# Kernel tuning notes

Hardware: AMD Instinct MI355X
Metric: run time of the kernel (lower is better)

The kernel has to match this reference:

```python
import jax, jax.numpy as jnp
import numpy as np

HIDDEN = 2048
N_HEADS = 8
N_KV_HEADS = 1
HEAD_DIM = 256
ROPE_THETA = 10000.0
B, S = 2, 2048


def setup_inputs() -> dict:
    key = jax.random.key(0)
    ks = jax.random.split(key, 6)
    sc = 0.02
    hidden_states = jax.random.normal(ks[0], (B, S, HIDDEN), dtype=jnp.float32)
    position_ids = jnp.broadcast_to(jnp.arange(S, dtype=jnp.int64 if jax.config.jax_enable_x64 else jnp.int32), (B, S))
    # additive causal mask: 0 on/below diagonal, large negative above
    causal = jnp.tril(jnp.ones((S, S), dtype=bool))
    attention_mask = jnp.where(causal, 0.0, -1e9).astype(jnp.float32)[None, None, :, :]
    attention_mask = jnp.broadcast_to(attention_mask, (B, 1, S, S))
    Wq = jax.random.normal(ks[1], (HIDDEN, N_HEADS * HEAD_DIM), dtype=jnp.float32) * sc
    Wk = jax.random.normal(ks[2], (HIDDEN, N_KV_HEADS * HEAD_DIM), dtype=jnp.float32) * sc
    Wv = jax.random.normal(ks[3], (HIDDEN, N_KV_HEADS * HEAD_DIM), dtype=jnp.float32) * sc
    Wo = jax.random.normal(ks[4], (N_HEADS * HEAD_DIM, HIDDEN), dtype=jnp.float32) * sc
    return {"hidden_states": hidden_states, "position_ids": position_ids,
            "attention_mask": attention_mask, "Wq": Wq, "Wk": Wk, "Wv": Wv, "Wo": Wo}


def _rotate_half(x):
    x1, x2 = jnp.split(x, 2, axis=-1)
    return jnp.concatenate([-x2, x1], axis=-1)


def _rope_cos_sin(position_ids, dtype):
    # inv_freq: [head_dim/2]
    inv_freq = 1.0 / (ROPE_THETA ** (jnp.arange(0, HEAD_DIM, 2, dtype=jnp.float32) / HEAD_DIM))
    # freqs: [B, S, head_dim/2]
    freqs = position_ids.astype(jnp.float32)[:, :, None] * inv_freq[None, None, :]
    emb = jnp.concatenate([freqs, freqs], axis=-1)  # [B, S, head_dim]
    return jnp.cos(emb).astype(dtype), jnp.sin(emb).astype(dtype)


def reference(hidden_states, position_ids, attention_mask, Wq, Wk, Wv, Wo):
    b, s, _ = hidden_states.shape
    # projections (bias=False)
    q = (hidden_states @ Wq).reshape(b, s, N_HEADS, HEAD_DIM).transpose(0, 2, 1, 3)      # [B,H,S,D]
    k = (hidden_states @ Wk).reshape(b, s, N_KV_HEADS, HEAD_DIM).transpose(0, 2, 1, 3)   # [B,Hk,S,D]
    v = (hidden_states @ Wv).reshape(b, s, N_KV_HEADS, HEAD_DIM).transpose(0, 2, 1, 3)
    cos, sin = _rope_cos_sin(position_ids, hidden_states.dtype)  # [B,S,D]
    cos, sin = cos[:, None], sin[:, None]  # [B,1,S,D]
    q = q * cos + _rotate_half(q) * sin
    k = k * cos + _rotate_half(k) * sin
    # repeat_kv for GQA
    n_rep = N_HEADS // N_KV_HEADS
    k = jnp.repeat(k, n_rep, axis=1)  # [B,H,S,D]
    v = jnp.repeat(v, n_rep, axis=1)
    scale = HEAD_DIM ** -0.5
    scores = jnp.einsum('bhqd,bhkd->bhqk', q, k) * scale + attention_mask
    attn_weights = jax.nn.softmax(scores.astype(jnp.float32), axis=-1).astype(q.dtype)
    attn_out = jnp.einsum('bhqk,bhkd->bhqd', attn_weights, v)
    attn_out = attn_out.transpose(0, 2, 1, 3).reshape(b, s, N_HEADS * HEAD_DIM)
    out = attn_out @ Wo
    return out, attn_weights
```

## Files before the change

kernel.cpp:

```cpp
#include <hip/hip_runtime.h>
#include <hip/hip_bf16.h>
#include <math.h>

typedef __attribute__((ext_vector_type(4))) float f32x4;
typedef __attribute__((ext_vector_type(8))) __bf16 bf16x8;
typedef __attribute__((ext_vector_type(8))) unsigned short u16x8;
typedef __attribute__((ext_vector_type(4))) unsigned short u16x4;

#define HID    2048
#define NHEADS 8
#define HDIM   256
#define SEQ    2048
#define BATCH  2
#define ROWS   (BATCH*SEQ)
#define QKVN   (NHEADS*HDIM + 2*HDIM)
#define NBH    (BATCH*NHEADS)

typedef __attribute__((address_space(1))) const void gvoid_t;
typedef __attribute__((address_space(3))) void lvoid_t;

__device__ __forceinline__ void gload16(const void* g, void* l){
  __builtin_amdgcn_global_load_lds((gvoid_t*)g, (lvoid_t*)l, 16, 0, 0);
}

__device__ __forceinline__ float bf2f(unsigned short u){
  union { unsigned int i; float f; } x; x.i = ((unsigned int)u) << 16; return x.f;
}
__device__ __forceinline__ unsigned short f2bf(float f){
  union { float f; unsigned int i; } x; x.f = f;
  unsigned int u = x.i;
  return (unsigned short)((u + 0x7FFFu + ((u >> 16) & 1u)) >> 16);
}

__global__ __launch_bounds__(256)
void k_f32_to_bf16(const float* __restrict__ src, unsigned short* __restrict__ dst){
  long i = ((long)blockIdx.x * 256 + threadIdx.x) * 16;
  f32x4 x0 = *(const f32x4*)(src + i);
  f32x4 x1 = *(const f32x4*)(src + i + 4);
  f32x4 x2 = *(const f32x4*)(src + i + 8);
  f32x4 x3 = *(const f32x4*)(src + i + 12);
  u16x8 w0, w1;
  #pragma unroll
  for (int j = 0; j < 4; ++j){
    w0[j]   = f2bf(x0[j]);
    w0[4+j] = f2bf(x1[j]);
    w1[j]   = f2bf(x2[j]);
    w1[4+j] = f2bf(x3[j]);
  }
  *(u16x8*)(dst + i)     = w0;
  *(u16x8*)(dst + i + 8) = w1;
}

__global__ __launch_bounds__(256)
void k_transpose(const float* __restrict__ src, unsigned short* __restrict__ dst,
                 int srcCols, int dstLd){
  __shared__ float t[32][33];
  int bx = blockIdx.x * 32;
  int by = blockIdx.y * 32;
  int tx = threadIdx.x & 31, ty = threadIdx.x >> 5;
  #pragma unroll
  for (int i = 0; i < 4; ++i){
    int rr = ty + i*8;
    t[rr][tx] = src[(long)(by + rr)*srcCols + bx + tx];
  }
  __syncthreads();
  #pragma unroll
  for (int i = 0; i < 4; ++i){
    int rr = ty + i*8;
    dst[(long)(bx + rr)*dstLd + by + tx] = f2bf(t[tx][rr]);
  }
}

__global__ __launch_bounds__(256)
void k_rope(const unsigned short* __restrict__ qkv, const int* __restrict__ pos_ids,
            unsigned short* __restrict__ Qb, unsigned short* __restrict__ Kb){
  int row = blockIdx.x;
  float pos = (float)pos_ids[row];
  int tid = threadIdx.x;
  const unsigned short* r = qkv + (long)row * QKVN;

  #pragma unroll
  for (int it = 0; it < 4; ++it){
    int p = it*256 + tid;
    int d = p & 127, h = p >> 7;
    int col = h*HDIM + d;
    float inv = exp2f((float)d * -0.10381025296523132f);
    float ang = pos * inv;
    float sn, cs; sincosf(ang, &sn, &cs);
    float x0 = bf2f(r[col]), x1 = bf2f(r[col + 128]);
    Qb[(long)row*HID + col]       = f2bf(x0*cs - x1*sn);
    Qb[(long)row*HID + col + 128] = f2bf(x1*cs + x0*sn);
  }
  if (tid < 128){
    int d = tid;
    float inv = exp2f((float)d * -0.10381025296523132f);
    float ang = pos * inv;
    float sn, cs; sincosf(ang, &sn, &cs);
    float x0 = bf2f(r[HID + d]), x1 = bf2f(r[HID + d + 128]);
    Kb[(long)row*HDIM + d]       = f2bf(x0*cs - x1*sn);
    Kb[(long)row*HDIM + d + 128] = f2bf(x1*cs + x0*sn);
  }
}

__global__ __launch_bounds__(256)
void k_vt(const unsigned short* __restrict__ qkvb, unsigned short* __restrict__ VT){
  __shared__ unsigned short t[32][34];
  int d0 = blockIdx.x * 32, s0 = blockIdx.y * 32, b = blockIdx.z;
  int tx = threadIdx.x & 31, ty = threadIdx.x >> 5;
  #pragma unroll
  for (int i = 0; i < 4; ++i){
    int rr = ty + i*8;
    t[rr][tx] = qkvb[(long)(b*SEQ + s0 + rr)*QKVN + HID + HDIM + d0 + tx];
  }
  __syncthreads();
  #pragma unroll
  for (int i = 0; i < 4; ++i){
    int dd = ty + i*8;
    VT[((long)b*HDIM + d0 + dd)*SEQ + s0 + tx] = t[tx][dd];
  }
}

__global__ __launch_bounds__(512, 4)
void k_fused(const unsigned short* __restrict__ Qb, const unsigned short* __restrict__ Kb,
             const unsigned short* __restrict__ VT, float* __restrict__ S,
             unsigned short* __restrict__ AOb){
  int bh = blockIdx.x, b = bh >> 3, h = bh & 7;
  int ss = 31 - (int)blockIdx.y;
  int qbase = ss * 64;
  int T = 2 * (ss + 1);

  float* Sh = S + (long)bh * SEQ * SEQ;
  const unsigned short* Qh = Qb + (long)b*SEQ*HID + (long)h*HDIM;
  const unsigned short* Kh = Kb + (long)b*SEQ*HDIM;
  const unsigned short* Vh = VT + (long)b*HDIM*SEQ;

  __shared__ unsigned short lK[2][32*256];
  __shared__ __bf16 lA[2][64*40];
  __shared__ float lWl[8][64];
  __shared__ float mli[64];

  int tid = threadIdx.x, lane = tid & 63, w = tid >> 6;
  int wr = w >> 1, wc = w & 1;

#define STAGE_K(kt_, buf_)                                                      \
  { _Pragma("unroll")                                                           \
    for (int t = 0; t < 2; ++t){                                                \
      int seg = w*2 + t;                                                        \
      int row = seg*2 + (lane >> 5);                                            \
      int cb  = ((lane & 31)*16) ^ ((row & 7) << 4);                            \
      gload16(Kh + (long)((kt_)*32 + row)*HDIM + (cb >> 1),                     \
              (char*)lK[buf_] + seg*1024);                                      \
    } }

#define QKT(buf_)                                                               \
  { _Pragma("unroll")                                                           \
    for (int kk = 0; kk < 8; ++kk){                                             \
      int rk = wc*16 + (lane & 15);                                             \
      bf16x8 bk = *(const bf16x8*)((const char*)lK[buf_] + rk*512 +             \
                   ((kk*64 + (lane >> 4)*16) ^ ((rk & 7) << 4)));               \
      accs = __builtin_amdgcn_mfma_f32_16x16x32_bf16(aq[kk], bk, accs, 0, 0, 0);\
    } }

  bf16x8 aq[8];
  {
    const unsigned short* qrow = Qh + (long)(qbase + wr*16 + (lane & 15))*HID + (lane >> 4)*8;
    #pragma unroll
    for (int kk = 0; kk < 8; ++kk)
      aq[kk] = *(const bf16x8*)(qrow + kk*32);
  }

  f32x4 accs;
  f32x4 acc_o[4][2];
  float oL[4];
  #pragma unroll
  for (int q = 0; q < 4; ++q){ accs[q] = 0.f; oL[q] = 0.f; }
  #pragma unroll
  for (int m = 0; m < 4; ++m)
    #pragma unroll
    for (int n = 0; n < 2; ++n)
      #pragma unroll
      for (int q = 0; q < 4; ++q) acc_o[m][n][q] = 0.f;

  STAGE_K(0, 0)
  STAGE_K(1, 1)
  asm volatile("s_waitcnt vmcnt(2)" ::: "memory");
  __builtin_amdgcn_s_barrier();
  for (int kt = 0; kt < T; ++kt){
    __builtin_amdgcn_s_setprio(1);
    QKT(kt & 1)
    __builtin_amdgcn_s_setprio(0);
    if (kt*32 + wc*16 + 15 <= qbase + wr*16){
      #pragma unroll
      for (int ri = 0; ri < 4; ++ri){
        int rowl = wr*16 + (lane >> 4)*4 + ri;
        int coll = wc*16 + (lane & 15);
        float e = __expf(accs[ri]*0.0625f - 8.0f);
        oL[ri] += e;
        lA[kt & 1][rowl*40 + coll] = (__bf16)e;
        accs[ri] = 0.f;
      }
    } else {
      #pragma unroll
      for (int ri = 0; ri < 4; ++ri){
        int rowl = wr*16 + (lane >> 4)*4 + ri;
        int coll = wc*16 + (lane & 15);
        float e = (kt*32 + coll <= qbase + rowl) ? __expf(accs[ri]*0.0625f - 8.0f) : 0.f;
        oL[ri] += e;
        lA[kt & 1][rowl*40 + coll] = (__bf16)e;
        accs[ri] = 0.f;
      }
    }
    bf16x8 vf0 = *(const bf16x8*)(Vh + (long)(w*32 +      (lane & 15))*SEQ + kt*32 + (lane >> 4)*8);
    bf16x8 vf1 = *(const bf16x8*)(Vh + (long)(w*32 + 16 + (lane & 15))*SEQ + kt*32 + (lane >> 4)*8);
    asm volatile("s_waitcnt lgkmcnt(0)" ::: "memory");
    asm volatile("s_waitcnt vmcnt(2)" ::: "memory");
    __builtin_amdgcn_s_barrier();
    if (kt + 2 < T) STAGE_K(kt + 2, kt & 1)
    __builtin_amdgcn_s_setprio(1);
    #pragma unroll
    for (int m2 = 0; m2 < 4; ++m2){
      int rq = m2*16 + (lane & 15);
      bf16x8 ap = *(const bf16x8*)&lA[kt & 1][rq*40 + (lane >> 4)*8];
      acc_o[m2][0] = __builtin_amdgcn_mfma_f32_16x16x32_bf16(ap, vf0, acc_o[m2][0], 0, 0, 0);
      acc_o[m2][1] = __builtin_amdgcn_mfma_f32_16x16x32_bf16(ap, vf1, acc_o[m2][1], 0, 0, 0);
    }
    __builtin_amdgcn_s_setprio(0);
  }

  #pragma unroll
  for (int ri = 0; ri < 4; ++ri){
    float v = oL[ri];
    #pragma unroll
    for (int off = 1; off < 16; off <<= 1) v += __shfl_xor(v, off);
    if ((lane & 15) == 0)
      lWl[w][wr*16 + (lane >> 4)*4 + ri] = v;
  }
  __syncthreads();
  if (tid < 64){
    int g = (tid >> 4) * 2;
    mli[tid] = 1.0f / (lWl[g][tid] + lWl[g+1][tid]);
  }
  __syncthreads();

  float ils[4];
  #pragma unroll
  for (int ri = 0; ri < 4; ++ri)
    ils[ri] = mli[wr*16 + (lane >> 4)*4 + ri];

  #pragma unroll
  for (int m2 = 0; m2 < 4; ++m2){
    #pragma unroll
    for (int ri = 0; ri < 4; ++ri){
      int row = m2*16 + (lane >> 4)*4 + ri;
      float il = mli[row];
      long gr = (long)b*SEQ + qbase + row;
      #pragma unroll
      for (int n = 0; n < 2; ++n){
        int col = w*32 + n*16 + (lane & 15);
        AOb[gr*HID + h*HDIM + col] = f2bf(acc_o[m2][n][ri] * il);
      }
    }
  }

  STAGE_K(0, 0)
  STAGE_K(1, 1)
  asm volatile("s_waitcnt vmcnt(2)" ::: "memory");
  __builtin_amdgcn_s_barrier();
  for (int kt = 0; kt < T; ++kt){
    __builtin_amdgcn_s_setprio(1);
    QKT(kt & 1)
    __builtin_amdgcn_s_setprio(0);
    if (kt*32 + wc*16 + 15 <= qbase + wr*16){
      #pragma unroll
      for (int ri = 0; ri < 4; ++ri){
        int rowl = wr*16 + (lane >> 4)*4 + ri;
        int coll = wc*16 + (lane & 15);
        Sh[(long)(qbase + rowl)*SEQ + kt*32 + coll] =
            __expf(accs[ri]*0.0625f - 8.0f) * ils[ri];
        accs[ri] = 0.f;
      }
    } else {
      #pragma unroll
      for (int ri = 0; ri < 4; ++ri){
        int rowl = wr*16 + (lane >> 4)*4 + ri;
        int coll = wc*16 + (lane & 15);
        float p = (kt*32 + coll <= qbase + rowl)
                  ? __expf(accs[ri]*0.0625f - 8.0f) * ils[ri] : 0.f;
        Sh[(long)(qbase + rowl)*SEQ + kt*32 + coll] = p;
        accs[ri] = 0.f;
      }
    }
    asm volatile("s_waitcnt vmcnt(4)" ::: "memory");
    __builtin_amdgcn_s_barrier();
    if (kt + 2 < T) STAGE_K(kt + 2, kt & 1)
  }

  {
    f32x4 z4; z4[0]=0.f; z4[1]=0.f; z4[2]=0.f; z4[3]=0.f;
    int row = qbase + (tid >> 3);
    for (int c = T*32 + (tid & 7)*4; c < SEQ; c += 32)
      *(f32x4*)&Sh[(long)row*SEQ + c] = z4;
  }
#undef STAGE_K
#undef QKT
}

template<int OUTF32>
__global__ __launch_bounds__(512, 1)
void gemm256(const unsigned short* __restrict__ A16, const unsigned short* __restrict__ BT,
             void* __restrict__ Cv, int lda, int ldb, int ldc, int K){
  constexpr int BM = 256, BN = 128, BK = 64;
  int m0 = blockIdx.x * BM, n0 = blockIdx.y * BN;

  __shared__ unsigned short lA[2][BM*BK];
  __shared__ unsigned short lB[2][BN*BK];

  int tid = threadIdx.x, lane = tid & 63, w = tid >> 6;
  int wr = w >> 1, wc = w & 1;
  int srow = lane >> 3;
  int vswz = ((lane & 7) ^ ((lane >> 3) & 7)) * 8;

  f32x4 acc[4][4];
  #pragma unroll
  for (int m = 0; m < 4; ++m)
    #pragma unroll
    for (int n = 0; n < 4; ++n)
      #pragma unroll
      for (int q = 0; q < 4; ++q) acc[m][n][q] = 0.f;

  int NT = K / BK;

#define STAGE256(kt_, buf_)                                                    \
  { int k0_ = (kt_) * BK;                                                      \
    _Pragma("unroll")                                                          \
    for (int t = 0; t < 4; ++t){                                               \
      int seg = w*4 + t;                                                       \
      const unsigned short* src = A16 + (long)(m0 + seg*8 + srow)*lda + k0_ + vswz; \
      gload16(src, (char*)lA[buf_] + seg*1024);                                \
    }                                                                          \
    _Pragma("unroll")                                                          \
    for (int t = 0; t < 2; ++t){                                               \
      int seg = w*2 + t;                                                       \
      const unsigned short* src = BT + (long)(n0 + seg*8 + srow)*ldb + k0_ + vswz; \
      gload16(src, (char*)lB[buf_] + seg*1024);                                \
    } }

  STAGE256(0, 0)
  STAGE256(1, 1)
  int cur = 0;

  for (int kt = 0; kt < NT; ++kt){
    if (kt < NT - 1) asm volatile("s_waitcnt vmcnt(6)" ::: "memory");
    else             asm volatile("s_waitcnt vmcnt(0)" ::: "memory");
    __builtin_amdgcn_s_barrier();

    const char* La = (const char*)lA[cur];
    const char* Lb = (const char*)lB[cur];
    __builtin_amdgcn_s_setprio(1);
    #pragma unroll
    for (int kk = 0; kk < 2; ++kk){
      bf16x8 af[4], bfr[4];
      #pragma unroll
      for (int m = 0; m < 4; ++m){
        int row = wr*64 + m*16 + (lane & 15);
        int kb = (kk*64 + (lane >> 4)*16) ^ ((row & 7) << 4);
        af[m] = *(const bf16x8*)(La + row*128 + kb);
      }
      #pragma unroll
      for (int n = 0; n < 4; ++n){
        int row = wc*64 + n*16 + (lane & 15);
        int kb = (kk*64 + (lane >> 4)*16) ^ ((row & 7) << 4);
        bfr[n] = *(const bf16x8*)(Lb + row*128 + kb);
      }
      #pragma unroll
      for (int m = 0; m < 4; ++m)
        #pragma unroll
        for (int n = 0; n < 4; ++n)
          acc[m][n] = __builtin_amdgcn_mfma_f32_16x16x32_bf16(af[m], bfr[n], acc[m][n], 0, 0, 0);
    }
    __builtin_amdgcn_s_setprio(0);
    __builtin_amdgcn_s_barrier();
    if (kt + 2 < NT) STAGE256(kt + 2, cur)
    cur ^= 1;
  }
#undef STAGE256

  #pragma unroll
  for (int m = 0; m < 4; ++m){
    #pragma unroll
    for (int ri = 0; ri < 4; ++ri){
      int orow = m0 + wr*64 + m*16 + (lane >> 4)*4 + ri;
      #pragma unroll
      for (int n = 0; n < 4; ++n){
        int ocol = n0 + wc*64 + n*16 + (lane & 15);
        float vv = acc[m][n][ri];
        if (OUTF32) ((float*)Cv)[(long)orow*ldc + ocol] = vv;
        else        ((unsigned short*)Cv)[(long)orow*ldc + ocol] = f2bf(vv);
      }
    }
  }
}

extern "C" void kernel_launch(void* const* d_in, const int* in_sizes, int n_in,
                              void* d_out, int out_size, void* d_ws, size_t ws_size,
                              hipStream_t stream){
  const float* hs  = (const float*)d_in[0];
  const int*   pos = (const int*)  d_in[1];
  const float* Wq  = (const float*)d_in[3];
  const float* Wk  = (const float*)d_in[4];
  const float* Wv  = (const float*)d_in[5];
  const float* Wo  = (const float*)d_in[6];

  float* out  = (float*)d_out;
  float* Sbuf = out + (long)ROWS * HID;

  unsigned short* wsp   = (unsigned short*)d_ws;
  unsigned short* hsb   = wsp;
  unsigned short* wqkvT = hsb   + (long)ROWS*HID;
  unsigned short* woT   = wqkvT + (long)QKVN*HID;
  unsigned short* qkvb  = woT   + (long)HID*HID;
  unsigned short* Qb    = qkvb  + (long)ROWS*QKVN;
  unsigned short* Kb    = Qb    + (long)ROWS*HID;
  unsigned short* VT    = Kb    + (long)ROWS*HDIM;
  unsigned short* AOb   = VT    + (long)BATCH*HDIM*SEQ;

  k_f32_to_bf16<<<(ROWS*HID)/(256*16), 256, 0, stream>>>(hs, hsb);
  k_transpose<<<dim3(HID/32,  HID/32), 256, 0, stream>>>(Wq, wqkvT, HID, HID);
  k_transpose<<<dim3(HDIM/32, HID/32), 256, 0, stream>>>(Wk, wqkvT + (long)HID*HID, HDIM, HID);
  k_transpose<<<dim3(HDIM/32, HID/32), 256, 0, stream>>>(Wv, wqkvT + (long)(HID+HDIM)*HID, HDIM, HID);
  k_transpose<<<dim3(HID/32,  HID/32), 256, 0, stream>>>(Wo, woT, HID, HID);

  gemm256<0><<<dim3(ROWS/256, QKVN/128), 512, 0, stream>>>(
      hsb, wqkvT, qkvb, HID, HID, QKVN, HID);

  k_rope<<<ROWS, 256, 0, stream>>>(qkvb, pos, Qb, Kb);
  k_vt<<<dim3(HDIM/32, SEQ/32, BATCH), 256, 0, stream>>>(qkvb, VT);

  k_fused<<<dim3(NBH, 32), 512, 0, stream>>>(Qb, Kb, VT, Sbuf, AOb);

  gemm256<1><<<dim3(ROWS/256, HID/128), 512, 0, stream>>>(
      AOb, woT, out, HID, HID, HID, HID);
}
```

Before: 318.4 us.

## Triple-buffer K tiles, prefetch V one step ahead, interleave block order

```diff
diff --git a/kernel.cpp b/kernel.cpp
--- a/kernel.cpp
+++ b/kernel.cpp
@@ -5,7 +5,6 @@
 typedef __attribute__((ext_vector_type(4))) float f32x4;
 typedef __attribute__((ext_vector_type(8))) __bf16 bf16x8;
 typedef __attribute__((ext_vector_type(8))) unsigned short u16x8;
-typedef __attribute__((ext_vector_type(4))) unsigned short u16x4;
 
 #define HID    2048
 #define NHEADS 8
@@ -125,7 +124,8 @@
              const unsigned short* __restrict__ VT, float* __restrict__ S,
              unsigned short* __restrict__ AOb){
   int bh = blockIdx.x, b = bh >> 3, h = bh & 7;
-  int ss = 31 - (int)blockIdx.y;
+  int y = (int)blockIdx.y;
+  int ss = (y < 16) ? (31 - y) : (y - 16);
   int qbase = ss * 64;
   int T = 2 * (ss + 1);
 
@@ -134,7 +134,7 @@
   const unsigned short* Kh = Kb + (long)b*SEQ*HDIM;
   const unsigned short* Vh = VT + (long)b*HDIM*SEQ;
 
-  __shared__ unsigned short lK[2][32*256];
+  __shared__ unsigned short lK[3][32*256];
   __shared__ __bf16 lA[2][64*40];
   __shared__ float lWl[8][64];
   __shared__ float mli[64];
@@ -168,6 +168,8 @@
     for (int kk = 0; kk < 8; ++kk)
       aq[kk] = *(const bf16x8*)(qrow + kk*32);
   }
+  const unsigned short* vb0 = Vh + (long)(w*32 +      (lane & 15))*SEQ + (lane >> 4)*8;
+  const unsigned short* vb1 = Vh + (long)(w*32 + 16 + (lane & 15))*SEQ + (lane >> 4)*8;
 
   f32x4 accs;
   f32x4 acc_o[4][2];
@@ -183,11 +185,22 @@
 
   STAGE_K(0, 0)
   STAGE_K(1, 1)
-  asm volatile("s_waitcnt vmcnt(2)" ::: "memory");
+  if (T > 2) STAGE_K(2, 2)
+  bf16x8 vc0 = *(const bf16x8*)(vb0);
+  bf16x8 vc1 = *(const bf16x8*)(vb1);
+  if (T > 2) asm volatile("s_waitcnt vmcnt(6)" ::: "memory");
+  else       asm volatile("s_waitcnt vmcnt(4)" ::: "memory");
   __builtin_amdgcn_s_barrier();
+
+  int bc = 0;
   for (int kt = 0; kt < T; ++kt){
+    bf16x8 vn0, vn1;
+    if (kt + 1 < T){
+      vn0 = *(const bf16x8*)(vb0 + (kt+1)*32);
+      vn1 = *(const bf16x8*)(vb1 + (kt+1)*32);
+    }
     __builtin_amdgcn_s_setprio(1);
-    QKT(kt & 1)
+    QKT(bc)
     __builtin_amdgcn_s_setprio(0);
     if (kt*32 + wc*16 + 15 <= qbase + wr*16){
       #pragma unroll
@@ -210,21 +223,24 @@
         accs[ri] = 0.f;
       }
     }
-    bf16x8 vf0 = *(const bf16x8*)(Vh + (long)(w*32 +      (lane & 15))*SEQ + kt*32 + (lane >> 4)*8);
-    bf16x8 vf1 = *(const bf16x8*)(Vh + (long)(w*32 + 16 + (lane & 15))*SEQ + kt*32 + (lane >> 4)*8);
     asm volatile("s_waitcnt lgkmcnt(0)" ::: "memory");
-    asm volatile("s_waitcnt vmcnt(2)" ::: "memory");
+    if (kt + 1 < T){
+      if (kt + 2 < T) asm volatile("s_waitcnt vmcnt(6)" ::: "memory");
+      else            asm volatile("s_waitcnt vmcnt(4)" ::: "memory");
+    }
     __builtin_amdgcn_s_barrier();
-    if (kt + 2 < T) STAGE_K(kt + 2, kt & 1)
+    if (kt + 3 < T) STAGE_K(kt + 3, bc)
     __builtin_amdgcn_s_setprio(1);
     #pragma unroll
     for (int m2 = 0; m2 < 4; ++m2){
       int rq = m2*16 + (lane & 15);
       bf16x8 ap = *(const bf16x8*)&lA[kt & 1][rq*40 + (lane >> 4)*8];
-      acc_o[m2][0] = __builtin_amdgcn_mfma_f32_16x16x32_bf16(ap, vf0, acc_o[m2][0], 0, 0, 0);
-      acc_o[m2][1] = __builtin_amdgcn_mfma_f32_16x16x32_bf16(ap, vf1, acc_o[m2][1], 0, 0, 0);
+      acc_o[m2][0] = __builtin_amdgcn_mfma_f32_16x16x32_bf16(ap, vc0, acc_o[m2][0], 0, 0, 0);
+      acc_o[m2][1] = __builtin_amdgcn_mfma_f32_16x16x32_bf16(ap, vc1, acc_o[m2][1], 0, 0, 0);
     }
     __builtin_amdgcn_s_setprio(0);
+    vc0 = vn0; vc1 = vn1;
+    bc = (bc == 2) ? 0 : bc + 1;
   }
 
   #pragma unroll
@@ -264,11 +280,15 @@
 
   STAGE_K(0, 0)
   STAGE_K(1, 1)
-  asm volatile("s_waitcnt vmcnt(2)" ::: "memory");
+  if (T > 2) STAGE_K(2, 2)
+  if (T > 2) asm volatile("s_waitcnt vmcnt(4)" ::: "memory");
+  else       asm volatile("s_waitcnt vmcnt(2)" ::: "memory");
   __builtin_amdgcn_s_barrier();
+
+  bc = 0;
   for (int kt = 0; kt < T; ++kt){
     __builtin_amdgcn_s_setprio(1);
-    QKT(kt & 1)
+    QKT(bc)
     __builtin_amdgcn_s_setprio(0);
     if (kt*32 + wc*16 + 15 <= qbase + wr*16){
       #pragma unroll
@@ -290,9 +310,18 @@
         accs[ri] = 0.f;
       }
     }
-    asm volatile("s_waitcnt vmcnt(4)" ::: "memory");
-    __builtin_amdgcn_s_barrier();
-    if (kt + 2 < T) STAGE_K(kt + 2, kt & 1)
+    if (kt + 1 < T){
+      if (kt == 0){
+        if (kt + 2 < T) asm volatile("s_waitcnt vmcnt(6)" ::: "memory");
+        else            asm volatile("s_waitcnt vmcnt(4)" ::: "memory");
+      } else {
+        if (kt + 2 < T) asm volatile("s_waitcnt vmcnt(10)" ::: "memory");
+        else            asm volatile("s_waitcnt vmcnt(8)" ::: "memory");
+      }
+      __builtin_amdgcn_s_barrier();
+      if (kt + 3 < T) STAGE_K(kt + 3, bc)
+    }
+    bc = (bc == 2) ? 0 : bc + 1;
   }
 
   {
```

Result: slower. 346.9 us (+9.0%).

## Shrink fused attention query tile to 32 rows with 256-thread blocks

Applied to the files above, without the earlier changes.

```diff
diff --git a/kernel.cpp b/kernel.cpp
--- a/kernel.cpp
+++ b/kernel.cpp
@@ -5,7 +5,6 @@
 typedef __attribute__((ext_vector_type(4))) float f32x4;
 typedef __attribute__((ext_vector_type(8))) __bf16 bf16x8;
 typedef __attribute__((ext_vector_type(8))) unsigned short u16x8;
-typedef __attribute__((ext_vector_type(4))) unsigned short u16x4;
 
 #define HID    2048
 #define NHEADS 8
@@ -120,14 +119,14 @@
   }
 }
 
-__global__ __launch_bounds__(512, 4)
+__global__ __launch_bounds__(256, 4)
 void k_fused(const unsigned short* __restrict__ Qb, const unsigned short* __restrict__ Kb,
              const unsigned short* __restrict__ VT, float* __restrict__ S,
              unsigned short* __restrict__ AOb){
   int bh = blockIdx.x, b = bh >> 3, h = bh & 7;
-  int ss = 31 - (int)blockIdx.y;
-  int qbase = ss * 64;
-  int T = 2 * (ss + 1);
+  int ss = 63 - (int)blockIdx.y;
+  int qbase = ss * 32;
+  int T = ss + 1;
 
   float* Sh = S + (long)bh * SEQ * SEQ;
   const unsigned short* Qh = Qb + (long)b*SEQ*HID + (long)h*HDIM;
@@ -135,17 +134,17 @@
   const unsigned short* Vh = VT + (long)b*HDIM*SEQ;
 
   __shared__ unsigned short lK[2][32*256];
-  __shared__ __bf16 lA[2][64*40];
-  __shared__ float lWl[8][64];
-  __shared__ float mli[64];
+  __shared__ __bf16 lA[2][32*40];
+  __shared__ float lWl[4][32];
+  __shared__ float mli[32];
 
   int tid = threadIdx.x, lane = tid & 63, w = tid >> 6;
-  int wr = w >> 1, wc = w & 1;
+  int wr = w & 1, wc = w >> 1;
 
 #define STAGE_K(kt_, buf_)                                                      \
   { _Pragma("unroll")                                                           \
-    for (int t = 0; t < 2; ++t){                                                \
-      int seg = w*2 + t;                                                        \
+    for (int t = 0; t < 4; ++t){                                                \
+      int seg = w*4 + t;                                                        \
       int row = seg*2 + (lane >> 5);                                            \
       int cb  = ((lane & 31)*16) ^ ((row & 7) << 4);                            \
       gload16(Kh + (long)((kt_)*32 + row)*HDIM + (cb >> 1),                     \
@@ -168,24 +167,34 @@
     for (int kk = 0; kk < 8; ++kk)
       aq[kk] = *(const bf16x8*)(qrow + kk*32);
   }
+  const unsigned short* vb[4];
+  #pragma unroll
+  for (int n = 0; n < 4; ++n)
+    vb[n] = Vh + (long)(w*64 + n*16 + (lane & 15))*SEQ + (lane >> 4)*8;
 
   f32x4 accs;
-  f32x4 acc_o[4][2];
+  f32x4 acc_o[2][4];
   float oL[4];
   #pragma unroll
   for (int q = 0; q < 4; ++q){ accs[q] = 0.f; oL[q] = 0.f; }
   #pragma unroll
-  for (int m = 0; m < 4; ++m)
-    #pragma unroll
-    for (int n = 0; n < 2; ++n)
+  for (int m = 0; m < 2; ++m)
+    #pragma unroll
+    for (int n = 0; n < 4; ++n)
       #pragma unroll
       for (int q = 0; q < 4; ++q) acc_o[m][n][q] = 0.f;
 
   STAGE_K(0, 0)
-  STAGE_K(1, 1)
-  asm volatile("s_waitcnt vmcnt(2)" ::: "memory");
+  if (T > 1) STAGE_K(1, 1)
+  if (T > 1) asm volatile("s_waitcnt vmcnt(4)" ::: "memory");
+  else       asm volatile("s_waitcnt vmcnt(0)" ::: "memory");
   __builtin_amdgcn_s_barrier();
+
   for (int kt = 0; kt < T; ++kt){
+    bf16x8 vf[4];
+    #pragma unroll
+    for (int n = 0; n < 4; ++n)
+      vf[n] = *(const bf16x8*)(vb[n] + kt*32);
     __builtin_amdgcn_s_setprio(1);
     QKT(kt & 1)
     __builtin_amdgcn_s_setprio(0);
@@ -210,19 +219,19 @@
         accs[ri] = 0.f;
       }
     }
-    bf16x8 vf0 = *(const bf16x8*)(Vh + (long)(w*32 +      (lane & 15))*SEQ + kt*32 + (lane >> 4)*8);
-    bf16x8 vf1 = *(const bf16x8*)(Vh + (long)(w*32 + 16 + (lane & 15))*SEQ + kt*32 + (lane >> 4)*8);
     asm volatile("s_waitcnt lgkmcnt(0)" ::: "memory");
-    asm volatile("s_waitcnt vmcnt(2)" ::: "memory");
+    if (kt + 1 < T)
+      asm volatile("s_waitcnt vmcnt(4)" ::: "memory");
     __builtin_amdgcn_s_barrier();
     if (kt + 2 < T) STAGE_K(kt + 2, kt & 1)
     __builtin_amdgcn_s_setprio(1);
     #pragma unroll
-    for (int m2 = 0; m2 < 4; ++m2){
+    for (int m2 = 0; m2 < 2; ++m2){
       int rq = m2*16 + (lane & 15);
       bf16x8 ap = *(const bf16x8*)&lA[kt & 1][rq*40 + (lane >> 4)*8];
-      acc_o[m2][0] = __builtin_amdgcn_mfma_f32_16x16x32_bf16(ap, vf0, acc_o[m2][0], 0, 0, 0);
-      acc_o[m2][1] = __builtin_amdgcn_mfma_f32_16x16x32_bf16(ap, vf1, acc_o[m2][1], 0, 0, 0);
+      #pragma unroll
+      for (int n = 0; n < 4; ++n)
+        acc_o[m2][n] = __builtin_amdgcn_mfma_f32_16x16x32_bf16(ap, vf[n], acc_o[m2][n], 0, 0, 0);
     }
     __builtin_amdgcn_s_setprio(0);
   }
@@ -236,9 +245,9 @@
       lWl[w][wr*16 + (lane >> 4)*4 + ri] = v;
   }
   __syncthreads();
-  if (tid < 64){
-    int g = (tid >> 4) * 2;
-    mli[tid] = 1.0f / (lWl[g][tid] + lWl[g+1][tid]);
+  if (tid < 32){
+    int g = tid >> 4;
+    mli[tid] = 1.0f / (lWl[g][tid] + lWl[g + 2][tid]);
   }
   __syncthreads();
 
@@ -248,24 +257,26 @@
     ils[ri] = mli[wr*16 + (lane >> 4)*4 + ri];
 
   #pragma unroll
-  for (int m2 = 0; m2 < 4; ++m2){
+  for (int m2 = 0; m2 < 2; ++m2){
     #pragma unroll
     for (int ri = 0; ri < 4; ++ri){
       int row = m2*16 + (lane >> 4)*4 + ri;
       float il = mli[row];
       long gr = (long)b*SEQ + qbase + row;
       #pragma unroll
-      for (int n = 0; n < 2; ++n){
-        int col = w*32 + n*16 + (lane & 15);
+      for (int n = 0; n < 4; ++n){
+        int col = w*64 + n*16 + (lane & 15);
         AOb[gr*HID + h*HDIM + col] = f2bf(acc_o[m2][n][ri] * il);
       }
     }
   }
 
   STAGE_K(0, 0)
-  STAGE_K(1, 1)
-  asm volatile("s_waitcnt vmcnt(2)" ::: "memory");
+  if (T > 1) STAGE_K(1, 1)
+  if (T > 1) asm volatile("s_waitcnt vmcnt(4)" ::: "memory");
+  else       asm volatile("s_waitcnt vmcnt(0)" ::: "memory");
   __builtin_amdgcn_s_barrier();
+
   for (int kt = 0; kt < T; ++kt){
     __builtin_amdgcn_s_setprio(1);
     QKT(kt & 1)
@@ -290,9 +301,11 @@
         accs[ri] = 0.f;
       }
     }
-    asm volatile("s_waitcnt vmcnt(4)" ::: "memory");
-    __builtin_amdgcn_s_barrier();
-    if (kt + 2 < T) STAGE_K(kt + 2, kt & 1)
+    if (kt + 1 < T){
+      asm volatile("s_waitcnt vmcnt(4)" ::: "memory");
+      __builtin_amdgcn_s_barrier();
+      if (kt + 2 < T) STAGE_K(kt + 2, kt & 1)
+    }
   }
 
   {
@@ -436,7 +449,7 @@
   k_rope<<<ROWS, 256, 0, stream>>>(qkvb, pos, Qb, Kb);
   k_vt<<<dim3(HDIM/32, SEQ/32, BATCH), 256, 0, stream>>>(qkvb, VT);
 
-  k_fused<<<dim3(NBH, 32), 512, 0, stream>>>(Qb, Kb, VT, Sbuf, AOb);
+  k_fused<<<dim3(NBH, 64), 256, 0, stream>>>(Qb, Kb, VT, Sbuf, AOb);
 
   gemm256<1><<<dim3(ROWS/256, HID/128), 512, 0, stream>>>(
       AOb, woT, out, HID, HID, HID, HID);
```

Measured after the change: 417.9 us. +31.3%, slower.
